# Performance work log

Hardware: AMD Instinct MI355X
Metric: run time of the kernel (lower is better)

Reference implementation:

```python
import jax, jax.numpy as jnp
import numpy as np

EPS_BN = 1e-5
EPS_W = 1e-8


def setup_inputs() -> dict:
    key = jax.random.key(0)
    ks = jax.random.split(key, 6)
    B, N, S, D1, D2 = 8, 8192, 2048, 128, 256
    Cin = D1 + D2  # 384
    return {
        "points_position": jax.random.normal(ks[0], (B, 3, N), jnp.float32),
        "sampled_points_position": jax.random.normal(ks[1], (B, 3, S), jnp.float32),
        "skip_points_feature": jax.random.normal(ks[2], (B, D1, N), jnp.float32),
        "sampled_points_feature": jax.random.normal(ks[3], (B, D2, S), jnp.float32),
        "W1": jax.random.normal(ks[4], (256, Cin), jnp.float32) * 0.05,
        "b1": jnp.zeros((256,), jnp.float32),
        "g1": jnp.ones((256,), jnp.float32),
        "beta1": jnp.zeros((256,), jnp.float32),
        "W2": jax.random.normal(ks[5], (128, 256), jnp.float32) * 0.05,
        "b2": jnp.zeros((128,), jnp.float32),
        "g2": jnp.ones((128,), jnp.float32),
        "beta2": jnp.zeros((128,), jnp.float32),
    }


def _bn_relu(x, g, b):
    # train-mode BatchNorm1d over (batch, points) per channel, x: [B,N,C]
    mean = jnp.mean(x, axis=(0, 1), keepdims=True)
    var = jnp.mean(jnp.square(x - mean), axis=(0, 1), keepdims=True)  # biased var
    return jax.nn.relu((x - mean) * jax.lax.rsqrt(var + EPS_BN) * g + b)


def reference(points_position, sampled_points_position, skip_points_feature,
              sampled_points_feature, W1, b1, g1, beta1, W2, b2, g2, beta2):
    pos = points_position.transpose(0, 2, 1)            # [B,N,3]
    spos = sampled_points_position.transpose(0, 2, 1)   # [B,S,3]
    sfeat = sampled_points_feature.transpose(0, 2, 1)   # [B,S,D2]

    # squared pairwise distance [B,N,S]
    d = (jnp.sum(pos * pos, axis=-1, keepdims=True)
         - 2.0 * jnp.einsum("bnc,bsc->bns", pos, spos)
         + jnp.sum(spos * spos, axis=-1)[:, None, :])

    # 3 nearest neighbors (smallest distances)
    neg_d3, idx = jax.lax.top_k(-d, 3)                  # [B,N,3]
    d3 = -neg_d3
    w = 1.0 / (d3 + EPS_W)
    w = w / jnp.sum(w, axis=-1, keepdims=True)          # [B,N,3]

    gathered = jax.vmap(lambda f, i: f[i])(sfeat, idx)  # [B,N,3,D2]
    interp = jnp.einsum("bnk,bnkd->bnd", w, gathered)   # [B,N,D2]

    feat = jnp.concatenate([skip_points_feature.transpose(0, 2, 1), interp], axis=-1)  # [B,N,D1+D2]

    h = _bn_relu(jnp.einsum("bnc,oc->bno", feat, W1) + b1, g1, beta1)  # [B,N,256]
    h = _bn_relu(jnp.einsum("bnc,oc->bno", h, W2) + b2, g2, beta2)     # [B,N,128]
    return h.transpose(0, 2, 1)                          # [B,128,N]
```

## Files before the change

### kernel.cpp

```cpp
#include <hip/hip_runtime.h>

constexpr int BATCH = 8;
constexpr int NPT   = 8192;
constexpr int NSMP  = 2048;
constexpr int D1C   = 128;
constexpr int D2C   = 256;
constexpr int CIN   = 384;
constexpr int C1    = 256;
constexpr int C2    = 128;
constexpr int BN_TOTAL = BATCH * NPT;

constexpr int WM = 128, WN = 64, WK = 32;
constexpr int NRB = BN_TOTAL / WM;

typedef __bf16 bf16x8 __attribute__((ext_vector_type(8)));
typedef short  s16x8  __attribute__((ext_vector_type(8)));
typedef float  f32x4  __attribute__((ext_vector_type(4)));

__device__ __forceinline__ unsigned short f2bf(float x) {
  unsigned u = __builtin_bit_cast(unsigned, x);
  u += 0x7fffu + ((u >> 16) & 1u);
  return (unsigned short)(u >> 16);
}
__device__ __forceinline__ float bf2f(unsigned short h) {
  return __builtin_bit_cast(float, (unsigned)h << 16);
}

__device__ __forceinline__ void gld_lds16(const void* g, void* l) {
  __builtin_amdgcn_global_load_lds(
      (const __attribute__((address_space(1))) void*)g,
      (__attribute__((address_space(3))) void*)l, 16, 0, 0);
}

__global__ void transpose_k(const float* __restrict__ in, float* __restrict__ out,
                            int rows, int cols, long inBatch, long outBatch) {
  __shared__ float tile[32][33];
  const float* inb = in + (size_t)blockIdx.z * inBatch;
  float* outb = out + (size_t)blockIdx.z * outBatch;
  int c0 = blockIdx.x * 32;
  int r0 = blockIdx.y * 32;
  int tx = threadIdx.x, ty = threadIdx.y;
#pragma unroll
  for (int i = 0; i < 32; i += 8) {
    int r = r0 + ty + i;
    tile[ty + i][tx] = inb[(size_t)r * cols + c0 + tx];
  }
  __syncthreads();
#pragma unroll
  for (int i = 0; i < 32; i += 8) {
    int c = c0 + ty + i;
    outb[(size_t)c * rows + r0 + tx] = tile[tx][ty + i];
  }
}

__global__ void skip_to_featB(const float* __restrict__ skip,
                              unsigned short* __restrict__ featB) {
  __shared__ float tile[32][33];
  int b = blockIdx.z;
  int n0 = blockIdx.x * 32;
  int d0 = blockIdx.y * 32;
  int tx = threadIdx.x, ty = threadIdx.y;
#pragma unroll
  for (int i = 0; i < 32; i += 8) {
    tile[ty + i][tx] = skip[((size_t)b * D1C + d0 + ty + i) * NPT + n0 + tx];
  }
  __syncthreads();
#pragma unroll
  for (int i = 0; i < 32; i += 8) {
    int n = n0 + ty + i;
    featB[((size_t)b * NPT + n) * CIN + d0 + tx] = f2bf(tile[tx][ty + i]);
  }
}

__global__ void wprep(const float* __restrict__ W, unsigned short* __restrict__ Wh,
                      int total) {
  int i = blockIdx.x * 256 + threadIdx.x;
  if (i >= total) return;
  Wh[i] = f2bf(W[i]);
}

__global__ void pack_spos(const float* __restrict__ spos, float* __restrict__ sposI,
                          float4* __restrict__ qs4) {
  int g = blockIdx.x * 256 + threadIdx.x;
  int b = g >> 11, s = g & (NSMP - 1);
  const float* sp = spos + (size_t)b * 3 * NSMP;
  float x = sp[s], y = sp[NSMP + s], z = sp[2 * NSMP + s];
  sposI[(size_t)g * 3 + 0] = x;
  sposI[(size_t)g * 3 + 1] = y;
  sposI[(size_t)g * 3 + 2] = z;
  qs4[g] = make_float4(-2.f * x, -2.f * y, -2.f * z,
                       fmaf(x, x, fmaf(y, y, z * z)));
}

constexpr int SEG = NSMP / 4;

__device__ __forceinline__ void ins_med3(float kf, float& k0, float& k1,
                                         float& k2, float& k3) {
  float o0 = k0, o1 = k1, o2 = k2;
  k0 = fminf(kf, o0);
  k1 = __builtin_amdgcn_fmed3f(kf, o0, o1);
  k2 = __builtin_amdgcn_fmed3f(kf, o1, o2);
  k3 = __builtin_amdgcn_fmed3f(kf, o2, k3);
}

__global__ __launch_bounds__(256) void knn_kernel(
    const float* __restrict__ pos,
    const float4* __restrict__ qs4g,
    const float* __restrict__ sposI,
    int* __restrict__ idx_out,
    float* __restrict__ wgt_out,
    int* __restrict__ flag_list,
    int* __restrict__ flag_count) {
  __shared__ float4 qs[NSMP];
  __shared__ float mk[4][4][64];

  int tid = threadIdx.x;
  int wave = tid >> 6, lane = tid & 63;
  int blk = blockIdx.x;
  int b = blk >> 7;
  int n = ((blk & 127) << 6) + lane;

  const float4* src = qs4g + (size_t)b * NSMP;
  for (int t = tid; t < NSMP; t += 256) qs[t] = src[t];
  __syncthreads();

  const float* pb = pos + (size_t)b * 3 * NPT;
  float px = pb[n], py = pb[NPT + n], pz = pb[2 * NPT + n];
  float pp = fmaf(px, px, fmaf(py, py, pz * pz));

  const float INF = __builtin_inff();
  float k0 = INF, k1 = INF, k2 = INF, k3 = INF;

  int s0 = wave * SEG;

#define KNN_STEP(Q, SS)                                                   \
  {                                                                       \
    float d = fmaf(px, (Q).x, fmaf(py, (Q).y, fmaf(pz, (Q).z, (Q).w + pp))); \
    unsigned ki = (__builtin_bit_cast(unsigned, d) & 0xFFFFF800u) |       \
                  (unsigned)(SS);                                         \
    ins_med3(__builtin_bit_cast(float, ki), k0, k1, k2, k3);              \
  }

  for (int t = 0; t < SEG; t += 4) {
    int s = s0 + t;
    float4 qa = qs[s], qb = qs[s + 1], qc = qs[s + 2], qd = qs[s + 3];
    KNN_STEP(qa, s + 0)
    KNN_STEP(qb, s + 1)
    KNN_STEP(qc, s + 2)
    KNN_STEP(qd, s + 3)
  }
#undef KNN_STEP

  mk[wave][0][lane] = k0; mk[wave][1][lane] = k1;
  mk[wave][2][lane] = k2; mk[wave][3][lane] = k3;
  __syncthreads();

  if (tid < 64) {
    float K0 = INF, K1 = INF, K2 = INF, K3 = INF;
#pragma unroll
    for (int w = 0; w < 4; w++)
#pragma unroll
      for (int sl = 0; sl < 4; sl++)
        ins_med3(mk[w][sl][tid], K0, K1, K2, K3);

    int p = blk * 64 + tid;
    int I0 = (int)(__builtin_bit_cast(unsigned, K0) & 0x7FFu);
    int I1 = (int)(__builtin_bit_cast(unsigned, K1) & 0x7FFu);
    int I2 = (int)(__builtin_bit_cast(unsigned, K2) & 0x7FFu);
    float d2m = __builtin_bit_cast(float, __builtin_bit_cast(unsigned, K2) & 0xFFFFF800u);
    float d3m = __builtin_bit_cast(float, __builtin_bit_cast(unsigned, K3) & 0xFFFFF800u);
    bool flag = (d3m - d2m) < 2e-3f * fmaxf(d3m, 0.f) + 1e-5f;
    if (flag) {
      int slot = atomicAdd(flag_count, 1);
      flag_list[slot] = p;
    }
    const float* q = sposI + (size_t)b * 3 * NSMP;
    double pxd = (double)px, pyd = (double)py, pzd = (double)pz;
    double dd[3]; int II[3] = {I0, I1, I2};
#pragma unroll
    for (int k = 0; k < 3; k++) {
      double dx = pxd - (double)q[3 * II[k]];
      double dy = pyd - (double)q[3 * II[k] + 1];
      double dz = pzd - (double)q[3 * II[k] + 2];
      dd[k] = dx * dx + dy * dy + dz * dz;
    }
    double w0 = 1.0 / (dd[0] + 1e-8);
    double w1 = 1.0 / (dd[1] + 1e-8);
    double w2 = 1.0 / (dd[2] + 1e-8);
    double inv = 1.0 / (w0 + w1 + w2);
    size_t o = (size_t)p * 3;
    idx_out[o + 0] = I0; idx_out[o + 1] = I1; idx_out[o + 2] = I2;
    wgt_out[o + 0] = (float)(w0 * inv);
    wgt_out[o + 1] = (float)(w1 * inv);
    wgt_out[o + 2] = (float)(w2 * inv);
  }
}

__device__ __forceinline__ bool dless(double d, int i, double D, int I) {
  return d < D || (d == D && i < I);
}
__device__ __forceinline__ void dins3(double d, int i,
                                      double& b0, double& b1, double& b2,
                                      int& i0, int& i1, int& i2) {
  if (dless(d, i, b2, i2)) {
    if (dless(d, i, b1, i1)) {
      b2 = b1; i2 = i1;
      if (dless(d, i, b0, i0)) { b1 = b0; i1 = i0; b0 = d; i0 = i; }
      else                     { b1 = d; i1 = i; }
    } else { b2 = d; i2 = i; }
  }
}

__global__ __launch_bounds__(256) void knn_fallback(
    const float* __restrict__ pos, const float* __restrict__ sposI,
    const int* __restrict__ flag_list, const int* __restrict__ flag_count,
    int* __restrict__ idx_out, float* __restrict__ wgt_out) {
  int wave = threadIdx.x >> 6, lane = threadIdx.x & 63;
  int gw = blockIdx.x * 4 + wave;
  int cnt = *flag_count;
  for (int t = gw; t < cnt; t += 1024) {
    int p = flag_list[t];
    int b = p >> 13, n = p & (NPT - 1);
    const float* pb = pos + (size_t)b * 3 * NPT;
    double px = (double)pb[n], py = (double)pb[NPT + n], pz = (double)pb[2 * NPT + n];
    const float* q = sposI + (size_t)b * 3 * NSMP;
    double b0 = 1e300, b1 = 1e300, b2 = 1e300;
    int i0 = 0x7FFFFFFF, i1 = 0x7FFFFFFF, i2 = 0x7FFFFFFF;
    for (int s = lane; s < NSMP; s += 64) {
      double dx = px - (double)q[3 * s];
      double dy = py - (double)q[3 * s + 1];
      double dz = pz - (double)q[3 * s + 2];
      double d = dx * dx + dy * dy + dz * dz;
      dins3(d, s, b0, b1, b2, i0, i1, i2);
    }
#pragma unroll
    for (int m = 1; m < 64; m <<= 1) {
      double o0 = __shfl_xor(b0, m, 64), o1 = __shfl_xor(b1, m, 64), o2 = __shfl_xor(b2, m, 64);
      int    j0 = __shfl_xor(i0, m, 64), j1 = __shfl_xor(i1, m, 64), j2 = __shfl_xor(i2, m, 64);
      dins3(o0, j0, b0, b1, b2, i0, i1, i2);
      dins3(o1, j1, b0, b1, b2, i0, i1, i2);
      dins3(o2, j2, b0, b1, b2, i0, i1, i2);
    }
    if (lane == 0) {
      double w0 = 1.0 / (b0 + 1e-8);
      double w1 = 1.0 / (b1 + 1e-8);
      double w2 = 1.0 / (b2 + 1e-8);
      double inv = 1.0 / (w0 + w1 + w2);
      size_t o = (size_t)p * 3;
      idx_out[o + 0] = i0; idx_out[o + 1] = i1; idx_out[o + 2] = i2;
      wgt_out[o + 0] = (float)(w0 * inv);
      wgt_out[o + 1] = (float)(w1 * inv);
      wgt_out[o + 2] = (float)(w2 * inv);
    }
  }
}

__global__ __launch_bounds__(256) void interp_kernel(
    const float* __restrict__ sfeatT,
    const int* __restrict__ idx,
    const float* __restrict__ wgt,
    unsigned short* __restrict__ featB) {
  int p = blockIdx.x;
  int c = threadIdx.x;
  int b = p >> 13;
  size_t o = (size_t)p * 3;
  int i0 = idx[o], i1 = idx[o + 1], i2 = idx[o + 2];
  float w0 = wgt[o], w1 = wgt[o + 1], w2 = wgt[o + 2];
  const float* base = sfeatT + (size_t)b * NSMP * D2C;
  float v = w0 * base[(size_t)i0 * D2C + c]
          + w1 * base[(size_t)i1 * D2C + c]
          + w2 * base[(size_t)i2 * D2C + c];
  featB[(size_t)p * CIN + D1C + c] = f2bf(v);
}

__global__ __launch_bounds__(64) void gemm1_wave(
    const unsigned short* __restrict__ featB,
    const unsigned short* __restrict__ W1h,
    const float* __restrict__ bias,
    unsigned short* __restrict__ Y1,
    float* __restrict__ part_s,
    float* __restrict__ part_q) {
  __shared__ __align__(16) unsigned short As[WM * WK];
  __shared__ __align__(16) unsigned short Bs[WN * WK];
  int lane = threadIdx.x;
  int m16 = lane & 15, quad = lane >> 4;
  int rb = blockIdx.x, cb = blockIdx.y;
  int row0 = rb * WM, col0 = cb * WN;
  int row16 = lane >> 2, col8 = (lane & 3) * 8;

  f32x4 acc[8][4];
#pragma unroll
  for (int j = 0; j < 4; j++) {
    float bj = bias[col0 + j * 16 + m16];
#pragma unroll
    for (int i = 0; i < 8; i++) acc[i][j] = f32x4{bj, bj, bj, bj};
  }

  for (int k0 = 0; k0 < CIN; k0 += WK) {
#pragma unroll
    for (int c = 0; c < 8; c++)
      gld_lds16(&featB[(size_t)(row0 + c * 16 + row16) * CIN + k0 + col8],
                &As[c * 16 * WK]);
#pragma unroll
    for (int c = 0; c < 4; c++)
      gld_lds16(&W1h[(size_t)(col0 + c * 16 + row16) * CIN + k0 + col8],
                &Bs[c * 16 * WK]);
    __syncthreads();

    bf16x8 a[8], bf[4];
#pragma unroll
    for (int i = 0; i < 8; i++)
      a[i] = __builtin_bit_cast(bf16x8, *(const s16x8*)&As[(i * 16 + m16) * WK + quad * 8]);
#pragma unroll
    for (int j = 0; j < 4; j++)
      bf[j] = __builtin_bit_cast(bf16x8, *(const s16x8*)&Bs[(j * 16 + m16) * WK + quad * 8]);
#pragma unroll
    for (int i = 0; i < 8; i++)
#pragma unroll
      for (int j = 0; j < 4; j++)
        acc[i][j] = __builtin_amdgcn_mfma_f32_16x16x32_bf16(a[i], bf[j], acc[i][j], 0, 0, 0);
    __syncthreads();
  }

#pragma unroll
  for (int j = 0; j < 4; j++) {
    int col = col0 + j * 16 + m16;
    float s = 0.f, q = 0.f;
#pragma unroll
    for (int i = 0; i < 8; i++)
#pragma unroll
      for (int r = 0; r < 4; r++) {
        float v = acc[i][j][r];
        Y1[(size_t)(row0 + i * 16 + quad * 4 + r) * C1 + col] = f2bf(v);
        s += v; q = fmaf(v, v, q);
      }
    s += __shfl_xor(s, 16, 64); s += __shfl_xor(s, 32, 64);
    q += __shfl_xor(q, 16, 64); q += __shfl_xor(q, 32, 64);
    if (quad == 0) {
      part_s[(size_t)col * NRB + rb] = s;
      part_q[(size_t)col * NRB + rb] = q;
    }
  }
}

__global__ __launch_bounds__(64) void gemm2_wave(
    const unsigned short* __restrict__ Y1,
    const float* __restrict__ scale1, const float* __restrict__ shift1,
    const unsigned short* __restrict__ W2h,
    const float* __restrict__ bias,
    unsigned short* __restrict__ Y2,
    float* __restrict__ part_s,
    float* __restrict__ part_q) {
  __shared__ __align__(16) unsigned short As[WM * WK];
  __shared__ __align__(16) unsigned short Bs[WN * WK];
  __shared__ float scs[C1], shs[C1];
  int lane = threadIdx.x;
  int m16 = lane & 15, quad = lane >> 4;
  int rb = blockIdx.x, cb = blockIdx.y;
  int row0 = rb * WM, col0 = cb * WN;
  int row16 = lane >> 2, col8 = (lane & 3) * 8;

  for (int t = lane; t < C1; t += 64) { scs[t] = scale1[t]; shs[t] = shift1[t]; }

  f32x4 acc[8][4];
#pragma unroll
  for (int j = 0; j < 4; j++) {
    float bj = bias[col0 + j * 16 + m16];
#pragma unroll
    for (int i = 0; i < 8; i++) acc[i][j] = f32x4{bj, bj, bj, bj};
  }
  __syncthreads();

  for (int k0 = 0; k0 < C1; k0 += WK) {
#pragma unroll
    for (int c = 0; c < 4; c++)
      gld_lds16(&W2h[(size_t)(col0 + c * 16 + row16) * C1 + k0 + col8],
                &Bs[c * 16 * WK]);
#pragma unroll
    for (int c = 0; c < 8; c++) {
      int row = c * 16 + row16;
      s16x8 v = *(const s16x8*)&Y1[(size_t)(row0 + row) * C1 + k0 + col8];
      unsigned short ov[8];
#pragma unroll
      for (int e = 0; e < 8; e++) {
        float x = bf2f((unsigned short)v[e]);
        float y = fmaxf(fmaf(x, scs[k0 + col8 + e], shs[k0 + col8 + e]), 0.f);
        ov[e] = f2bf(y);
      }
      *(s16x8*)&As[row * WK + col8] = *(const s16x8*)ov;
    }
    __syncthreads();

    bf16x8 a[8], bf[4];
#pragma unroll
    for (int i = 0; i < 8; i++)
      a[i] = __builtin_bit_cast(bf16x8, *(const s16x8*)&As[(i * 16 + m16) * WK + quad * 8]);
#pragma unroll
    for (int j = 0; j < 4; j++)
      bf[j] = __builtin_bit_cast(bf16x8, *(const s16x8*)&Bs[(j * 16 + m16) * WK + quad * 8]);
#pragma unroll
    for (int i = 0; i < 8; i++)
#pragma unroll
      for (int j = 0; j < 4; j++)
        acc[i][j] = __builtin_amdgcn_mfma_f32_16x16x32_bf16(a[i], bf[j], acc[i][j], 0, 0, 0);
    __syncthreads();
  }

#pragma unroll
  for (int j = 0; j < 4; j++) {
    int col = col0 + j * 16 + m16;
    float s = 0.f, q = 0.f;
#pragma unroll
    for (int i = 0; i < 8; i++)
#pragma unroll
      for (int r = 0; r < 4; r++) {
        float v = acc[i][j][r];
        Y2[(size_t)(row0 + i * 16 + quad * 4 + r) * C2 + col] = f2bf(v);
        s += v; q = fmaf(v, v, q);
      }
    s += __shfl_xor(s, 16, 64); s += __shfl_xor(s, 32, 64);
    q += __shfl_xor(q, 16, 64); q += __shfl_xor(q, 32, 64);
    if (quad == 0) {
      part_s[(size_t)col * NRB + rb] = s;
      part_q[(size_t)col * NRB + rb] = q;
    }
  }
}

__global__ __launch_bounds__(256) void bn_reduce_coef(
    const float* __restrict__ part_s, const float* __restrict__ part_q, int nrb,
    const float* __restrict__ g, const float* __restrict__ beta,
    float* __restrict__ scale, float* __restrict__ shift) {
  int ch = blockIdx.x;
  int tid = threadIdx.x;
  float s = 0.f, q = 0.f;
  for (int t = tid; t < nrb; t += 256) {
    s += part_s[(size_t)ch * nrb + t];
    q += part_q[(size_t)ch * nrb + t];
  }
#pragma unroll
  for (int m = 1; m < 64; m <<= 1) {
    s += __shfl_xor(s, m, 64);
    q += __shfl_xor(q, m, 64);
  }
  __shared__ float ls[4], lq[4];
  int wave = tid >> 6;
  if ((tid & 63) == 0) { ls[wave] = s; lq[wave] = q; }
  __syncthreads();
  if (tid == 0) {
    s = ls[0] + ls[1] + ls[2] + ls[3];
    q = lq[0] + lq[1] + lq[2] + lq[3];
    const float invBN = 1.0f / (float)BN_TOTAL;
    float mean = s * invBN;
    float var = q * invBN - mean * mean;
    float sc = g[ch] / sqrtf(var + 1e-5f);
    scale[ch] = sc;
    shift[ch] = beta[ch] - mean * sc;
  }
}

__global__ void final_kernel(const unsigned short* __restrict__ Y2,
                             const float* __restrict__ scale, const float* __restrict__ shift,
                             float* __restrict__ out) {
  __shared__ float tile[32][33];
  int b = blockIdx.z;
  int n0 = blockIdx.x * 32;
  int c0 = blockIdx.y * 32;
  int tx = threadIdx.x, ty = threadIdx.y;
  float sc = scale[c0 + tx];
  float sh = shift[c0 + tx];
#pragma unroll
  for (int i = 0; i < 32; i += 8) {
    int n = n0 + ty + i;
    float v = bf2f(Y2[((size_t)b * NPT + n) * C2 + c0 + tx]);
    tile[ty + i][tx] = fmaxf(fmaf(v, sc, sh), 0.f);
  }
  __syncthreads();
#pragma unroll
  for (int i = 0; i < 32; i += 8) {
    int c = c0 + ty + i;
    out[((size_t)b * C2 + c) * NPT + n0 + tx] = tile[tx][ty + i];
  }
}

extern "C" void kernel_launch(void* const* d_in, const int* in_sizes, int n_in,
                              void* d_out, int out_size, void* d_ws, size_t ws_size,
                              hipStream_t stream) {
  (void)in_sizes; (void)n_in; (void)out_size; (void)ws_size;
  const float* pos   = (const float*)d_in[0];
  const float* spos  = (const float*)d_in[1];
  const float* skip  = (const float*)d_in[2];
  const float* sfeat = (const float*)d_in[3];
  const float* W1    = (const float*)d_in[4];
  const float* b1    = (const float*)d_in[5];
  const float* g1    = (const float*)d_in[6];
  const float* beta1 = (const float*)d_in[7];
  const float* W2    = (const float*)d_in[8];
  const float* b2    = (const float*)d_in[9];
  const float* g2    = (const float*)d_in[10];
  const float* beta2 = (const float*)d_in[11];
  float* out = (float*)d_out;

  float* ws = (float*)d_ws;
  size_t off = 0;
  float* sfeatT  = ws + off; off += (size_t)BATCH * NSMP * D2C;
  unsigned short* featB = (unsigned short*)(ws + off); off += (size_t)BN_TOTAL * CIN / 2;
  unsigned short* Y1    = (unsigned short*)(ws + off); off += (size_t)BN_TOTAL * C1 / 2;
  unsigned short* Y2    = (unsigned short*)(ws + off); off += (size_t)BN_TOTAL * C2 / 2;
  unsigned short* W1h   = (unsigned short*)(ws + off); off += (size_t)C1 * CIN / 2;
  unsigned short* W2h   = (unsigned short*)(ws + off); off += (size_t)C2 * C1 / 2;
  int*   knn_idx = (int*)(ws + off); off += (size_t)BN_TOTAL * 3;
  float* knn_w   = ws + off; off += (size_t)BN_TOTAL * 3;
  float* sposI   = ws + off; off += (size_t)BATCH * NSMP * 3;
  float4* qs4    = (float4*)(ws + off); off += (size_t)BATCH * NSMP * 4;
  int* flag_list = (int*)(ws + off); off += (size_t)BN_TOTAL;
  float* part1_s = ws + off; off += (size_t)C1 * NRB;
  float* part1_q = ws + off; off += (size_t)C1 * NRB;
  float* part2_s = ws + off; off += (size_t)C2 * NRB;
  float* part2_q = ws + off; off += (size_t)C2 * NRB;
  float* stats   = ws + off; off += 2048;
  int*   flag_count = (int*)stats;
  float* scale1 = stats + 256, *shift1 = stats + 512;
  float* scale2 = stats + 768, *shift2 = stats + 1024;

  hipMemsetAsync(flag_count, 0, sizeof(int), stream);

  dim3 tb(32, 8);
  transpose_k<<<dim3(NSMP / 32, D2C / 32, BATCH), tb, 0, stream>>>(
      sfeat, sfeatT, D2C, NSMP, (long)D2C * NSMP, (long)NSMP * D2C);
  wprep<<<(C1 * CIN + 255) / 256, 256, 0, stream>>>(W1, W1h, C1 * CIN);
  wprep<<<(C2 * C1 + 255) / 256, 256, 0, stream>>>(W2, W2h, C2 * C1);
  skip_to_featB<<<dim3(NPT / 32, D1C / 32, BATCH), tb, 0, stream>>>(skip, featB);

  pack_spos<<<BATCH * NSMP / 256, 256, 0, stream>>>(spos, sposI, qs4);
  knn_kernel<<<BN_TOTAL / 64, 256, 0, stream>>>(pos, qs4, sposI, knn_idx, knn_w,
                                                flag_list, flag_count);
  knn_fallback<<<256, 256, 0, stream>>>(pos, sposI, flag_list, flag_count,
                                        knn_idx, knn_w);
  interp_kernel<<<BN_TOTAL, 256, 0, stream>>>(sfeatT, knn_idx, knn_w, featB);

  gemm1_wave<<<dim3(NRB, C1 / WN), 64, 0, stream>>>(
      featB, W1h, b1, Y1, part1_s, part1_q);
  bn_reduce_coef<<<C1, 256, 0, stream>>>(part1_s, part1_q, NRB, g1, beta1, scale1, shift1);

  gemm2_wave<<<dim3(NRB, C2 / WN), 64, 0, stream>>>(
      Y1, scale1, shift1, W2h, b2, Y2, part2_s, part2_q);
  bn_reduce_coef<<<C2, 256, 0, stream>>>(part2_s, part2_q, NRB, g2, beta2, scale2, shift2);

  final_kernel<<<dim3(NPT / 32, C2 / 32, BATCH), tb, 0, stream>>>(Y2, scale2, shift2, out);
}
```

Baseline: 304.3 us.

## Restructure GEMMs to 4-wave 128x128 tiles, stream KNN queries from global

Both GEMMs move from single-wave 128x64 tiles to 256-thread blocks with 128x128 tiles split across four waves. This raises operand reuse per LDS load, and gemm2 now computes all 128 output channels in one block, so the BN1-apply work on Y1 is done once instead of twice. BN partial sums are now kept per half-block. The KNN kernel no longer stages the query table in LDS and instead reads it from global memory with wave-uniform addresses, unrolled by 8. The interp kernel handles 16 points per block, and the two weight-prep launches are merged into one. The KNN change trades LDS reads for scalar or cached global loads, which may not be cheaper.

```diff
diff --git a/kernel.cpp b/kernel.cpp
--- a/kernel.cpp
+++ b/kernel.cpp
@@ -10,8 +10,9 @@
 constexpr int C2    = 128;
 constexpr int BN_TOTAL = BATCH * NPT;
 
-constexpr int WM = 128, WN = 64, WK = 32;
-constexpr int NRB = BN_TOTAL / WM;
+constexpr int BM = 128, BK = 32;
+constexpr int NRB = BN_TOTAL / BM;
+constexpr int NRW = NRB * 2;
 
 typedef __bf16 bf16x8 __attribute__((ext_vector_type(8)));
 typedef short  s16x8  __attribute__((ext_vector_type(8)));
@@ -72,11 +73,11 @@
   }
 }
 
-__global__ void wprep(const float* __restrict__ W, unsigned short* __restrict__ Wh,
-                      int total) {
+__global__ void wprep_both(const float* __restrict__ W1, unsigned short* __restrict__ W1h,
+                           const float* __restrict__ W2, unsigned short* __restrict__ W2h) {
   int i = blockIdx.x * 256 + threadIdx.x;
-  if (i >= total) return;
-  Wh[i] = f2bf(W[i]);
+  if (i < C1 * CIN) W1h[i] = f2bf(W1[i]);
+  if (i < C2 * C1)  W2h[i] = f2bf(W2[i]);
 }
 
 __global__ void pack_spos(const float* __restrict__ spos, float* __restrict__ sposI,
@@ -111,7 +112,6 @@
     float* __restrict__ wgt_out,
     int* __restrict__ flag_list,
     int* __restrict__ flag_count) {
-  __shared__ float4 qs[NSMP];
   __shared__ float mk[4][4][64];
 
   int tid = threadIdx.x;
@@ -120,10 +120,6 @@
   int b = blk >> 7;
   int n = ((blk & 127) << 6) + lane;
 
-  const float4* src = qs4g + (size_t)b * NSMP;
-  for (int t = tid; t < NSMP; t += 256) qs[t] = src[t];
-  __syncthreads();
-
   const float* pb = pos + (size_t)b * 3 * NPT;
   float px = pb[n], py = pb[NPT + n], pz = pb[2 * NPT + n];
   float pp = fmaf(px, px, fmaf(py, py, pz * pz));
@@ -132,22 +128,22 @@
   float k0 = INF, k1 = INF, k2 = INF, k3 = INF;
 
   int s0 = wave * SEG;
+  const float4* qseg = qs4g + (size_t)b * NSMP + __builtin_amdgcn_readfirstlane(s0);
 
 #define KNN_STEP(Q, SS)                                                   \
   {                                                                       \
-    float d = fmaf(px, (Q).x, fmaf(py, (Q).y, fmaf(pz, (Q).z, (Q).w + pp))); \
-    unsigned ki = (__builtin_bit_cast(unsigned, d) & 0xFFFFF800u) |       \
-                  (unsigned)(SS);                                         \
-    ins_med3(__builtin_bit_cast(float, ki), k0, k1, k2, k3);              \
-  }
-
-  for (int t = 0; t < SEG; t += 4) {
-    int s = s0 + t;
-    float4 qa = qs[s], qb = qs[s + 1], qc = qs[s + 2], qd = qs[s + 3];
-    KNN_STEP(qa, s + 0)
-    KNN_STEP(qb, s + 1)
-    KNN_STEP(qc, s + 2)
-    KNN_STEP(qd, s + 3)
+    float d_ = fmaf(px, (Q).x, fmaf(py, (Q).y, fmaf(pz, (Q).z, (Q).w + pp))); \
+    unsigned ki_ = (__builtin_bit_cast(unsigned, d_) & 0xFFFFF800u) |     \
+                   (unsigned)(SS);                                        \
+    ins_med3(__builtin_bit_cast(float, ki_), k0, k1, k2, k3);             \
+  }
+
+  for (int t = 0; t < SEG; t += 8) {
+    float4 qv[8];
+#pragma unroll
+    for (int u = 0; u < 8; u++) qv[u] = qseg[t + u];
+#pragma unroll
+    for (int u = 0; u < 8; u++) KNN_STEP(qv[u], s0 + t + u)
   }
 #undef KNN_STEP
 
@@ -255,95 +251,103 @@
   }
 }
 
+constexpr int IPB = 16;
 __global__ __launch_bounds__(256) void interp_kernel(
     const float* __restrict__ sfeatT,
     const int* __restrict__ idx,
     const float* __restrict__ wgt,
     unsigned short* __restrict__ featB) {
-  int p = blockIdx.x;
   int c = threadIdx.x;
-  int b = p >> 13;
-  size_t o = (size_t)p * 3;
-  int i0 = idx[o], i1 = idx[o + 1], i2 = idx[o + 2];
-  float w0 = wgt[o], w1 = wgt[o + 1], w2 = wgt[o + 2];
+  int p0 = blockIdx.x * IPB;
+  int b = p0 >> 13;
   const float* base = sfeatT + (size_t)b * NSMP * D2C;
-  float v = w0 * base[(size_t)i0 * D2C + c]
-          + w1 * base[(size_t)i1 * D2C + c]
-          + w2 * base[(size_t)i2 * D2C + c];
-  featB[(size_t)p * CIN + D1C + c] = f2bf(v);
-}
-
-__global__ __launch_bounds__(64) void gemm1_wave(
+#pragma unroll 4
+  for (int pi = 0; pi < IPB; pi++) {
+    int p = p0 + pi;
+    size_t o = (size_t)p * 3;
+    int i0 = idx[o], i1 = idx[o + 1], i2 = idx[o + 2];
+    float w0 = wgt[o], w1 = wgt[o + 1], w2 = wgt[o + 2];
+    float v = w0 * base[(size_t)i0 * D2C + c]
+            + w1 * base[(size_t)i1 * D2C + c]
+            + w2 * base[(size_t)i2 * D2C + c];
+    featB[(size_t)p * CIN + D1C + c] = f2bf(v);
+  }
+}
+
+__global__ __launch_bounds__(256) void gemm1_mw(
     const unsigned short* __restrict__ featB,
     const unsigned short* __restrict__ W1h,
     const float* __restrict__ bias,
     unsigned short* __restrict__ Y1,
     float* __restrict__ part_s,
     float* __restrict__ part_q) {
-  __shared__ __align__(16) unsigned short As[WM * WK];
-  __shared__ __align__(16) unsigned short Bs[WN * WK];
-  int lane = threadIdx.x;
+  __shared__ __align__(16) unsigned short As[BM * BK];
+  __shared__ __align__(16) unsigned short Bs[BM * BK];
+  int tid = threadIdx.x;
+  int lane = tid & 63, w = tid >> 6;
+  int wr = w >> 1, wc = w & 1;
   int m16 = lane & 15, quad = lane >> 4;
-  int rb = blockIdx.x, cb = blockIdx.y;
-  int row0 = rb * WM, col0 = cb * WN;
-  int row16 = lane >> 2, col8 = (lane & 3) * 8;
-
-  f32x4 acc[8][4];
+  int cb = blockIdx.x, rb = blockIdx.y;
+  int row0 = rb * BM, col0 = cb * BM;
+  int srow = lane >> 2, scol8 = (lane & 3) * 8;
+
+  f32x4 acc[4][4];
 #pragma unroll
   for (int j = 0; j < 4; j++) {
-    float bj = bias[col0 + j * 16 + m16];
-#pragma unroll
-    for (int i = 0; i < 8; i++) acc[i][j] = f32x4{bj, bj, bj, bj};
-  }
-
-  for (int k0 = 0; k0 < CIN; k0 += WK) {
-#pragma unroll
-    for (int c = 0; c < 8; c++)
-      gld_lds16(&featB[(size_t)(row0 + c * 16 + row16) * CIN + k0 + col8],
-                &As[c * 16 * WK]);
-#pragma unroll
-    for (int c = 0; c < 4; c++)
-      gld_lds16(&W1h[(size_t)(col0 + c * 16 + row16) * CIN + k0 + col8],
-                &Bs[c * 16 * WK]);
+    float bj = bias[col0 + wc * 64 + j * 16 + m16];
+#pragma unroll
+    for (int i = 0; i < 4; i++) acc[i][j] = f32x4{bj, bj, bj, bj};
+  }
+
+  for (int k0 = 0; k0 < CIN; k0 += BK) {
+#pragma unroll
+    for (int kq = 0; kq < 2; kq++) {
+      int ar = 32 * w + 16 * kq + srow;
+      int lb = __builtin_amdgcn_readfirstlane((32 * w + 16 * kq) * BK);
+      gld_lds16(&featB[(size_t)(row0 + ar) * CIN + k0 + scol8], &As[lb]);
+      gld_lds16(&W1h[(size_t)(col0 + ar) * CIN + k0 + scol8], &Bs[lb]);
+    }
     __syncthreads();
 
-    bf16x8 a[8], bf[4];
-#pragma unroll
-    for (int i = 0; i < 8; i++)
-      a[i] = __builtin_bit_cast(bf16x8, *(const s16x8*)&As[(i * 16 + m16) * WK + quad * 8]);
+    bf16x8 a[4], bb[4];
+#pragma unroll
+    for (int i = 0; i < 4; i++)
+      a[i] = __builtin_bit_cast(bf16x8,
+          *(const s16x8*)&As[(wr * 64 + i * 16 + m16) * BK + quad * 8]);
 #pragma unroll
     for (int j = 0; j < 4; j++)
-      bf[j] = __builtin_bit_cast(bf16x8, *(const s16x8*)&Bs[(j * 16 + m16) * WK + quad * 8]);
-#pragma unroll
-    for (int i = 0; i < 8; i++)
+      bb[j] = __builtin_bit_cast(bf16x8,
+          *(const s16x8*)&Bs[(wc * 64 + j * 16 + m16) * BK + quad * 8]);
+#pragma unroll
+    for (int i = 0; i < 4; i++)
 #pragma unroll
       for (int j = 0; j < 4; j++)
-        acc[i][j] = __builtin_amdgcn_mfma_f32_16x16x32_bf16(a[i], bf[j], acc[i][j], 0, 0, 0);
+        acc[i][j] = __builtin_amdgcn_mfma_f32_16x16x32_bf16(a[i], bb[j], acc[i][j], 0, 0, 0);
     __syncthreads();
   }
 
 #pragma unroll
   for (int j = 0; j < 4; j++) {
-    int col = col0 + j * 16 + m16;
+    int col = col0 + wc * 64 + j * 16 + m16;
     float s = 0.f, q = 0.f;
 #pragma unroll
-    for (int i = 0; i < 8; i++)
+    for (int i = 0; i < 4; i++)
 #pragma unroll
       for (int r = 0; r < 4; r++) {
         float v = acc[i][j][r];
-        Y1[(size_t)(row0 + i * 16 + quad * 4 + r) * C1 + col] = f2bf(v);
+        Y1[(size_t)(row0 + wr * 64 + i * 16 + quad * 4 + r) * C1 + col] = f2bf(v);
         s += v; q = fmaf(v, v, q);
       }
     s += __shfl_xor(s, 16, 64); s += __shfl_xor(s, 32, 64);
     q += __shfl_xor(q, 16, 64); q += __shfl_xor(q, 32, 64);
     if (quad == 0) {
-      part_s[(size_t)col * NRB + rb] = s;
-      part_q[(size_t)col * NRB + rb] = q;
-    }
-  }
-}
-
-__global__ __launch_bounds__(64) void gemm2_wave(
+      part_s[(size_t)col * NRW + rb * 2 + wr] = s;
+      part_q[(size_t)col * NRW + rb * 2 + wr] = q;
+    }
+  }
+}
+
+__global__ __launch_bounds__(256) void gemm2_mw(
     const unsigned short* __restrict__ Y1,
     const float* __restrict__ scale1, const float* __restrict__ shift1,
     const unsigned short* __restrict__ W2h,
@@ -351,78 +355,80 @@
     unsigned short* __restrict__ Y2,
     float* __restrict__ part_s,
     float* __restrict__ part_q) {
-  __shared__ __align__(16) unsigned short As[WM * WK];
-  __shared__ __align__(16) unsigned short Bs[WN * WK];
+  __shared__ __align__(16) unsigned short As[BM * BK];
+  __shared__ __align__(16) unsigned short Bs[BM * BK];
   __shared__ float scs[C1], shs[C1];
-  int lane = threadIdx.x;
+  int tid = threadIdx.x;
+  int lane = tid & 63, w = tid >> 6;
+  int wr = w >> 1, wc = w & 1;
   int m16 = lane & 15, quad = lane >> 4;
-  int rb = blockIdx.x, cb = blockIdx.y;
-  int row0 = rb * WM, col0 = cb * WN;
-  int row16 = lane >> 2, col8 = (lane & 3) * 8;
-
-  for (int t = lane; t < C1; t += 64) { scs[t] = scale1[t]; shs[t] = shift1[t]; }
-
-  f32x4 acc[8][4];
+  int rb = blockIdx.x;
+  int row0 = rb * BM, col0 = 0;
+  int srow = lane >> 2, scol8 = (lane & 3) * 8;
+
+  scs[tid] = scale1[tid]; shs[tid] = shift1[tid];
+
+  f32x4 acc[4][4];
 #pragma unroll
   for (int j = 0; j < 4; j++) {
-    float bj = bias[col0 + j * 16 + m16];
-#pragma unroll
-    for (int i = 0; i < 8; i++) acc[i][j] = f32x4{bj, bj, bj, bj};
+    float bj = bias[col0 + wc * 64 + j * 16 + m16];
+#pragma unroll
+    for (int i = 0; i < 4; i++) acc[i][j] = f32x4{bj, bj, bj, bj};
   }
   __syncthreads();
 
-  for (int k0 = 0; k0 < C1; k0 += WK) {
-#pragma unroll
-    for (int c = 0; c < 4; c++)
-      gld_lds16(&W2h[(size_t)(col0 + c * 16 + row16) * C1 + k0 + col8],
-                &Bs[c * 16 * WK]);
-#pragma unroll
-    for (int c = 0; c < 8; c++) {
-      int row = c * 16 + row16;
-      s16x8 v = *(const s16x8*)&Y1[(size_t)(row0 + row) * C1 + k0 + col8];
+  for (int k0 = 0; k0 < C1; k0 += BK) {
+#pragma unroll
+    for (int kq = 0; kq < 2; kq++) {
+      int ar = 32 * w + 16 * kq + srow;
+      int lb = __builtin_amdgcn_readfirstlane((32 * w + 16 * kq) * BK);
+      gld_lds16(&W2h[(size_t)(col0 + ar) * C1 + k0 + scol8], &Bs[lb]);
+      s16x8 v = *(const s16x8*)&Y1[(size_t)(row0 + ar) * C1 + k0 + scol8];
       unsigned short ov[8];
 #pragma unroll
       for (int e = 0; e < 8; e++) {
         float x = bf2f((unsigned short)v[e]);
-        float y = fmaxf(fmaf(x, scs[k0 + col8 + e], shs[k0 + col8 + e]), 0.f);
+        float y = fmaxf(fmaf(x, scs[k0 + scol8 + e], shs[k0 + scol8 + e]), 0.f);
         ov[e] = f2bf(y);
       }
-      *(s16x8*)&As[row * WK + col8] = *(const s16x8*)ov;
+      *(s16x8*)&As[ar * BK + scol8] = *(const s16x8*)ov;
     }
     __syncthreads();
 
-    bf16x8 a[8], bf[4];
-#pragma unroll
-    for (int i = 0; i < 8; i++)
-      a[i] = __builtin_bit_cast(bf16x8, *(const s16x8*)&As[(i * 16 + m16) * WK + quad * 8]);
+    bf16x8 a[4], bb[4];
+#pragma unroll
+    for (int i = 0; i < 4; i++)
+      a[i] = __builtin_bit_cast(bf16x8,
+          *(const s16x8*)&As[(wr * 64 + i * 16 + m16) * BK + quad * 8]);
 #pragma unroll
     for (int j = 0; j < 4; j++)
-      bf[j] = __builtin_bit_cast(bf16x8, *(const s16x8*)&Bs[(j * 16 + m16) * WK + quad * 8]);
-#pragma unroll
-    for (int i = 0; i < 8; i++)
+      bb[j] = __builtin_bit_cast(bf16x8,
+          *(const s16x8*)&Bs[(wc * 64 + j * 16 + m16) * BK + quad * 8]);
+#pragma unroll
+    for (int i = 0; i < 4; i++)
 #pragma unroll
       for (int j = 0; j < 4; j++)
-        acc[i][j] = __builtin_amdgcn_mfma_f32_16x16x32_bf16(a[i], bf[j], acc[i][j], 0, 0, 0);
+        acc[i][j] = __builtin_amdgcn_mfma_f32_16x16x32_bf16(a[i], bb[j], acc[i][j], 0, 0, 0);
     __syncthreads();
   }
 
 #pragma unroll
   for (int j = 0; j < 4; j++) {
-    int col = col0 + j * 16 + m16;
+    int col = col0 + wc * 64 + j * 16 + m16;
     float s = 0.f, q = 0.f;
 #pragma unroll
-    for (int i = 0; i < 8; i++)
+    for (int i = 0; i < 4; i++)
 #pragma unroll
       for (int r = 0; r < 4; r++) {
         float v = acc[i][j][r];
-        Y2[(size_t)(row0 + i * 16 + quad * 4 + r) * C2 + col] = f2bf(v);
+        Y2[(size_t)(row0 + wr * 64 + i * 16 + quad * 4 + r) * C2 + col] = f2bf(v);
         s += v; q = fmaf(v, v, q);
       }
     s += __shfl_xor(s, 16, 64); s += __shfl_xor(s, 32, 64);
     q += __shfl_xor(q, 16, 64); q += __shfl_xor(q, 32, 64);
     if (quad == 0) {
-      part_s[(size_t)col * NRB + rb] = s;
-      part_q[(size_t)col * NRB + rb] = q;
+      part_s[(size_t)col * NRW + rb * 2 + wr] = s;
+      part_q[(size_t)col * NRW + rb * 2 + wr] = q;
     }
   }
 }
@@ -514,10 +520,10 @@
   float* sposI   = ws + off; off += (size_t)BATCH * NSMP * 3;
   float4* qs4    = (float4*)(ws + off); off += (size_t)BATCH * NSMP * 4;
   int* flag_list = (int*)(ws + off); off += (size_t)BN_TOTAL;
-  float* part1_s = ws + off; off += (size_t)C1 * NRB;
-  float* part1_q = ws + off; off += (size_t)C1 * NRB;
-  float* part2_s = ws + off; off += (size_t)C2 * NRB;
-  float* part2_q = ws + off; off += (size_t)C2 * NRB;
+  float* part1_s = ws + off; off += (size_t)C1 * NRW;
+  float* part1_q = ws + off; off += (size_t)C1 * NRW;
+  float* part2_s = ws + off; off += (size_t)C2 * NRW;
+  float* part2_q = ws + off; off += (size_t)C2 * NRW;
   float* stats   = ws + off; off += 2048;
   int*   flag_count = (int*)stats;
   float* scale1 = stats + 256, *shift1 = stats + 512;
@@ -528,8 +534,7 @@
   dim3 tb(32, 8);
   transpose_k<<<dim3(NSMP / 32, D2C / 32, BATCH), tb, 0, stream>>>(
       sfeat, sfeatT, D2C, NSMP, (long)D2C * NSMP, (long)NSMP * D2C);
-  wprep<<<(C1 * CIN + 255) / 256, 256, 0, stream>>>(W1, W1h, C1 * CIN);
-  wprep<<<(C2 * C1 + 255) / 256, 256, 0, stream>>>(W2, W2h, C2 * C1);
+  wprep_both<<<(C1 * CIN + 255) / 256, 256, 0, stream>>>(W1, W1h, W2, W2h);
   skip_to_featB<<<dim3(NPT / 32, D1C / 32, BATCH), tb, 0, stream>>>(skip, featB);
 
   pack_spos<<<BATCH * NSMP / 256, 256, 0, stream>>>(spos, sposI, qs4);
@@ -537,15 +542,15 @@
                                                 flag_list, flag_count);
   knn_fallback<<<256, 256, 0, stream>>>(pos, sposI, flag_list, flag_count,
                                         knn_idx, knn_w);
-  interp_kernel<<<BN_TOTAL, 256, 0, stream>>>(sfeatT, knn_idx, knn_w, featB);
-
-  gemm1_wave<<<dim3(NRB, C1 / WN), 64, 0, stream>>>(
+  interp_kernel<<<BN_TOTAL / IPB, 256, 0, stream>>>(sfeatT, knn_idx, knn_w, featB);
+
+  gemm1_mw<<<dim3(C1 / BM, NRB), 256, 0, stream>>>(
       featB, W1h, b1, Y1, part1_s, part1_q);
-  bn_reduce_coef<<<C1, 256, 0, stream>>>(part1_s, part1_q, NRB, g1, beta1, scale1, shift1);
-
-  gemm2_wave<<<dim3(NRB, C2 / WN), 64, 0, stream>>>(
+  bn_reduce_coef<<<C1, 256, 0, stream>>>(part1_s, part1_q, NRW, g1, beta1, scale1, shift1);
+
+  gemm2_mw<<<NRB, 256, 0, stream>>>(
       Y1, scale1, shift1, W2h, b2, Y2, part2_s, part2_q);
-  bn_reduce_coef<<<C2, 256, 0, stream>>>(part2_s, part2_q, NRB, g2, beta2, scale2, shift2);
+  bn_reduce_coef<<<C2, 256, 0, stream>>>(part2_s, part2_q, NRW, g2, beta2, scale2, shift2);
 
   final_kernel<<<dim3(NPT / 32, C2 / 32, BATCH), tb, 0, stream>>>(Y2, scale2, shift2, out);
 }
```

New measurement: 288.3 us. 1.06x faster.
